# Optimization experiments

Measured on AMD Instinct MI355X. Metric: run time of the kernel, lower is better.

Reference implementation:

```python
import jax, jax.numpy as jnp
import numpy as np

K = 3
EPS = 1e-5
HID = 48
NB = 3


def conv2d(x, w, b):
    # x: NCHW, w: OIHW, 3x3 SAME conv stride 1
    y = jax.lax.conv_general_dilated(x, w, (1, 1), 'SAME',
                                     dimension_numbers=('NCHW', 'OIHW', 'NCHW'))
    return y + b[None, :, None, None]


def inorm(x):
    # InstanceNorm2d(affine=False): per-(n,c) spatial mean/var, biased var
    m = jnp.mean(x, axis=(2, 3), keepdims=True)
    v = jnp.var(x, axis=(2, 3), keepdims=True)
    return (x - m) * jax.lax.rsqrt(v + EPS)


def prelu(x, a):
    return jnp.where(x >= 0, x, a * x)


def basic_block(x, w, b, a):
    y = conv2d(x, w, b)
    y = inorm(y)
    y = prelu(y, a)
    y = inorm(y)
    return y + x


def maxpool2(x):
    n, c, h, w = x.shape
    return x.reshape(n, c, h // 2, 2, w // 2, 2).max(axis=(3, 5))


def upsample_bilinear8(x):
    # bilinear, scale_factor=8, align_corners=True
    n, c, h, w = x.shape
    H, W = h * 8, w * 8

    def coords(s, O):
        src = jnp.arange(O, dtype=jnp.float32) * (s - 1) / (O - 1)
        i0 = jnp.floor(src).astype(jnp.int32)
        i1 = jnp.minimum(i0 + 1, s - 1)
        return i0, i1, src - i0

    r0, r1, fr = coords(h, H)
    x = x[:, :, r0, :] * (1 - fr)[None, None, :, None] + x[:, :, r1, :] * fr[None, None, :, None]
    c0, c1, fc = coords(w, W)
    x = x[:, :, :, c0] * (1 - fc)[None, None, None, :] + x[:, :, :, c1] * fc[None, None, None, :]
    return x


def apply_kernel(x, kernel):
    # kernel: [n, k*k, h, w]; softmax over the k*k taps, reflect-pad unfold weighted sum
    kernel = jax.nn.softmax(kernel, axis=1)
    n, c, h, w = x.shape
    xp = jnp.pad(x, ((0, 0), (0, 0), (1, 1), (1, 1)), mode='reflect')
    patches = jnp.stack([xp[:, :, dy:dy + h, dx:dx + w]
                         for dy in range(K) for dx in range(K)], axis=0)  # [9,n,c,h,w]
    return jnp.einsum('pnchw,nphw->nchw', patches, kernel)


def setup_inputs() -> dict:
    key = jax.random.key(0)
    ks = jax.random.split(key, 12)
    f = jnp.float32
    inp = {
        'x': jax.random.normal(ks[0], (4, HID, 256, 256), dtype=f),
        'x_': jax.random.normal(ks[1], (4, HID, 256, 256), dtype=f),
        'pre1_w': jax.random.normal(ks[2], (NB, HID, HID, 3, 3), dtype=f) * 0.05,
        'pre1_b': jax.random.normal(ks[3], (NB, HID), dtype=f) * 0.05,
        'pre1_a': jnp.full((NB,), 0.25, dtype=f),
        'pre2_w': jax.random.normal(ks[4], (NB, HID, HID, 3, 3), dtype=f) * 0.05,
        'pre2_b': jax.random.normal(ks[5], (NB, HID), dtype=f) * 0.05,
        'pre2_a': jnp.full((NB,), 0.25, dtype=f),
        'prek_w1': jax.random.normal(ks[6], (HID, HID, 3, 3), dtype=f) * 0.05,
        'prek_b1': jax.random.normal(ks[7], (HID,), dtype=f) * 0.05,
        'prek_a': jnp.float32(0.25),
        'prek_w2': jax.random.normal(ks[8], (K * K, HID, 3, 3), dtype=f) * 0.05,
        'prek_b2': jax.random.normal(ks[9], (K * K,), dtype=f) * 0.05,
    }
    return inp


def reference(x, x_, pre1_w, pre1_b, pre1_a, pre2_w, pre2_b, pre2_a,
              prek_w1, prek_b1, prek_a, prek_w2, prek_b2):
    # F.interpolate(scale_factor=0.25, mode='nearest') == stride-4 subsample
    x1 = x_[:, :, ::4, ::4]
    for i in range(NB):
        x1 = basic_block(x1, pre1_w[i], pre1_b[i], pre1_a[i])
    x1 = maxpool2(x1)
    for i in range(NB):
        x1 = basic_block(x1, pre2_w[i], pre2_b[i], pre2_a[i])
    y = conv2d(x1, prek_w1, prek_b1)
    y = inorm(y)
    y = prelu(y, prek_a)
    skernel = conv2d(y, prek_w2, prek_b2)  # [n, k*k, H/8, W/8]
    kernel = upsample_bilinear8(skernel)   # [n, k*k, H, W]
    return apply_kernel(x, kernel)
```

## Files before the change

### kernel.cpp

```cpp
#include <hip/hip_runtime.h>
#include <cmath>

#define HIDC 48

__device__ __forceinline__ void block_meanvar1024(float s, float s2, float* red,
                                                  float cntinv, float& m, float& v)
{
#pragma unroll
    for (int off = 32; off > 0; off >>= 1) {
        s  += __shfl_down(s, off);
        s2 += __shfl_down(s2, off);
    }
    int wid  = threadIdx.x >> 6;
    int lane = threadIdx.x & 63;
    if (lane == 0) { red[wid] = s; red[16 + wid] = s2; }
    __syncthreads();
    if (threadIdx.x == 0) {
        float ts = 0.f, ts2 = 0.f;
#pragma unroll
        for (int i = 0; i < 16; ++i) { ts += red[i]; ts2 += red[16 + i]; }
        red[32] = ts; red[33] = ts2;
    }
    __syncthreads();
    float mean = red[32] * cntinv;
    m = mean;
    v = red[33] * cntinv - mean * mean;
    __syncthreads();
}

template <int H, int W, int ROWS, int COG, int CPS, int PXT, int NCH>
__global__ __launch_bounds__(ROWS*(W/PXT)) void conv_tile(
    const float* __restrict__ in,
    const float* __restrict__ wgt,
    float* __restrict__ out)
{
    constexpr int THREADS = ROWS * (W / PXT);
    constexpr int NPIX = H * W;
    constexpr int PW   = W + 4;
    constexpr int CHSZ = (ROWS + 2) * PW;
    constexpr int LSZ  = CPS * CHSZ;
    constexpr int TXN  = W / PXT;
    constexpr int NS   = NCH / CPS;
    constexpr int LPT  = (LSZ + THREADS - 1) / THREADS;

    __shared__ float plane[2][LSZ];

    const int t    = threadIdx.x;
    const int cg   = blockIdx.x;
    const int rt   = blockIdx.y;
    const int z    = blockIdx.z;
    const int half = z & 1;
    const int n    = z >> 1;
    const int COUT = gridDim.x * COG;
    const int co0  = cg * COG;
    const int cin0 = half * NCH;
    const int tx   = t % TXN;
    const int ty   = t / TXN;
    const int x0   = tx * PXT;
    const int r0   = rt * ROWS;
    const size_t OSTRIDE = (size_t)4 * COUT * NPIX;

    float acc[COG][PXT];
#pragma unroll
    for (int co = 0; co < COG; ++co)
#pragma unroll
        for (int p = 0; p < PXT; ++p) acc[co][p] = 0.f;

    const float* inb = in + ((size_t)n * 48 + cin0) * NPIX;

    int off[LPT];
#pragma unroll
    for (int k = 0; k < LPT; ++k) {
        int i = t + k * THREADS;
        off[k] = -1;
        if (i < LSZ) {
            int ch  = i / CHSZ;
            int rem = i % CHSZ;
            int ly  = rem / PW, lx = rem % PW;
            int gy  = r0 + ly - 1, gx = lx - 1;
            if (gy >= 0 && gy < H && gx >= 0 && gx < W)
                off[k] = ch * NPIX + gy * W + gx;
        }
    }

    float pref[LPT];
#pragma unroll
    for (int k = 0; k < LPT; ++k)
        pref[k] = (off[k] >= 0) ? inb[off[k]] : 0.f;

    int buf = 0;
    for (int s = 0; s < NS; ++s) {
        float cur[LPT];
#pragma unroll
        for (int k = 0; k < LPT; ++k) cur[k] = pref[k];
        if (s + 1 < NS) {
            const float* nb = inb + (size_t)(s + 1) * CPS * NPIX;
#pragma unroll
            for (int k = 0; k < LPT; ++k)
                pref[k] = (off[k] >= 0) ? nb[off[k]] : 0.f;
        }
#pragma unroll
        for (int k = 0; k < LPT; ++k) {
            int i = t + k * THREADS;
            if (i < LSZ) plane[buf][i] = cur[k];
        }
        __syncthreads();

#pragma unroll
        for (int c = 0; c < CPS; ++c) {
            const float* P = &plane[buf][c * CHSZ];
            float wv[COG][9];
#pragma unroll
            for (int co = 0; co < COG; ++co)
#pragma unroll
                for (int k = 0; k < 9; ++k)
                    wv[co][k] = wgt[((size_t)(co0 + co) * 48 + cin0 + s * CPS + c) * 9 + k];
            float vr[3][PXT + 2];
            if constexpr (PXT == 2) {
#pragma unroll
                for (int r = 0; r < 3; ++r) {
                    float2 a = *(const float2*)(P + (ty + r) * PW + x0);
                    float2 b = *(const float2*)(P + (ty + r) * PW + x0 + 2);
                    vr[r][0] = a.x; vr[r][1] = a.y; vr[r][2] = b.x; vr[r][3] = b.y;
                }
            } else {
#pragma unroll
                for (int r = 0; r < 3; ++r)
#pragma unroll
                    for (int j = 0; j < PXT + 2; ++j)
                        vr[r][j] = P[(ty + r) * PW + x0 + j];
            }
#pragma unroll
            for (int co = 0; co < COG; ++co)
#pragma unroll
                for (int p = 0; p < PXT; ++p) {
                    float s0 = vr[0][p]     * wv[co][0] + vr[0][p + 1] * wv[co][1]
                             + vr[0][p + 2] * wv[co][2] + vr[1][p]     * wv[co][3]
                             + vr[1][p + 1] * wv[co][4] + vr[1][p + 2] * wv[co][5]
                             + vr[2][p]     * wv[co][6] + vr[2][p + 1] * wv[co][7]
                             + vr[2][p + 2] * wv[co][8];
                    acc[co][p] += s0;
                }
        }
        buf ^= 1;
    }

#pragma unroll
    for (int co = 0; co < COG; ++co) {
        float* op = out + half * OSTRIDE
                  + (((size_t)n * COUT + co0 + co) * H + r0 + ty) * W + x0;
        if (PXT == 2) {
            *(float2*)op = make_float2(acc[co][0], acc[co][1]);
        } else {
#pragma unroll
            for (int p = 0; p < PXT; ++p) op[p] = acc[co][p];
        }
    }
}

template <int NPIX, int MODE, int POOL>
__global__ __launch_bounds__(1024) void norm_block(
    const float* __restrict__ c0,
    const float* __restrict__ c1,
    const float* __restrict__ res,
    const float* __restrict__ aptr,
    float* __restrict__ out)
{
    constexpr int TY = NPIX / 1024;
    constexpr bool VEC = (TY == 4) && (POOL == 0);
    __shared__ float red[34];
    const int t  = threadIdx.x;
    const int co = blockIdx.x;
    const int n  = blockIdx.y;
    const size_t base = ((size_t)n * 48 + co) * NPIX;
    constexpr float cntinv = 1.f / (float)NPIX;

    float acc[TY];
    size_t q = 0;
    if constexpr (POOL) {
        const int i = t >> 5, j = t & 31;
        q = base + (size_t)i * 128 + j * 2;
        float2 a0 = *(const float2*)(c0 + q);
        float2 a1 = *(const float2*)(c0 + q + 64);
        float2 b0 = *(const float2*)(c1 + q);
        float2 b1 = *(const float2*)(c1 + q + 64);
        acc[0] = a0.x + b0.x; acc[1] = a0.y + b0.y;
        acc[2] = a1.x + b1.x; acc[3] = a1.y + b1.y;
    } else if constexpr (VEC) {
        q = base + (size_t)t * 4;
        float4 a4 = *(const float4*)(c0 + q);
        float4 b4 = *(const float4*)(c1 + q);
        acc[0] = a4.x + b4.x; acc[1] = a4.y + b4.y;
        acc[2] = a4.z + b4.z; acc[3] = a4.w + b4.w;
    } else {
#pragma unroll
        for (int r = 0; r < TY; ++r)
            acc[r] = c0[base + t + r * 1024] + c1[base + t + r * 1024];
    }

    {
        float s = 0.f, s2 = 0.f;
#pragma unroll
        for (int r = 0; r < TY; ++r) { s += acc[r]; s2 += acc[r] * acc[r]; }
        float m, v;
        block_meanvar1024(s, s2, red, cntinv, m, v);
        float rr = rsqrtf(v + 1e-5f);
#pragma unroll
        for (int r = 0; r < TY; ++r) acc[r] = (acc[r] - m) * rr;
    }

    const float a = aptr[0];
#pragma unroll
    for (int r = 0; r < TY; ++r) acc[r] = acc[r] >= 0.f ? acc[r] : a * acc[r];

    if (MODE == 0) {
        float s = 0.f, s2 = 0.f;
#pragma unroll
        for (int r = 0; r < TY; ++r) { s += acc[r]; s2 += acc[r] * acc[r]; }
        float m, v;
        block_meanvar1024(s, s2, red, cntinv, m, v);
        float rr = rsqrtf(v + 1e-5f);
        if constexpr (POOL) {
            float2 r0v = *(const float2*)(res + q);
            float2 r1v = *(const float2*)(res + q + 64);
            acc[0] = (acc[0] - m) * rr + r0v.x;
            acc[1] = (acc[1] - m) * rr + r0v.y;
            acc[2] = (acc[2] - m) * rr + r1v.x;
            acc[3] = (acc[3] - m) * rr + r1v.y;
        } else if constexpr (VEC) {
            float4 r4 = *(const float4*)(res + q);
            acc[0] = (acc[0] - m) * rr + r4.x;
            acc[1] = (acc[1] - m) * rr + r4.y;
            acc[2] = (acc[2] - m) * rr + r4.z;
            acc[3] = (acc[3] - m) * rr + r4.w;
        } else {
#pragma unroll
            for (int r = 0; r < TY; ++r)
                acc[r] = (acc[r] - m) * rr + res[base + t + r * 1024];
        }
    }

    if constexpr (POOL) {
        out[(((size_t)n * 48 + co) << 10) + t] =
            fmaxf(fmaxf(acc[0], acc[1]), fmaxf(acc[2], acc[3]));
    } else if constexpr (VEC) {
        *(float4*)(out + q) = make_float4(acc[0], acc[1], acc[2], acc[3]);
    } else {
#pragma unroll
        for (int r = 0; r < TY; ++r) out[base + t + r * 1024] = acc[r];
    }
}

__global__ __launch_bounds__(256) void downsample4(const float* __restrict__ xin,
                                                   float* __restrict__ o)
{
    int idx = blockIdx.x * 256 + threadIdx.x;
    int j = idx & 63;
    int i = (idx >> 6) & 63;
    int nc = idx >> 12;
    o[idx] = xin[((size_t)nc * 256 + i * 4) * 256 + j * 4];
}

__global__ __launch_bounds__(256) void apply_fused(const float* __restrict__ x,
                                                   const float* __restrict__ sk0,
                                                   const float* __restrict__ sk1,
                                                   const float* __restrict__ kb2,
                                                   float* __restrict__ out)
{
    __shared__ float skr[9][2][32];
    __shared__ float kvs[9][256];
    const int bx = blockIdx.x;
    const int n  = bx >> 2;
    const int cg = bx & 3;
    const int h  = blockIdx.y;
    const int t  = threadIdx.x;

    const int wq = t & 63;
    const int cl = t >> 6;
    const int w4 = wq * 4;
    const int hm  = (h == 0) ? 1 : h - 1;
    const int hp  = (h == 255) ? 254 : h + 1;
    const int c0ch = cg * 12 + cl * 3;
    const float* xb = x + ((size_t)n * HIDC + c0ch) * 65536;
    float* ob = out + ((size_t)n * HIDC + c0ch) * 65536;

    float4 F[3][3];
#pragma unroll
    for (int c = 0; c < 3; ++c) {
        const float* xp = xb + (size_t)c * 65536;
        F[c][0] = *(const float4*)(xp + hm * 256 + w4);
        F[c][1] = *(const float4*)(xp + h  * 256 + w4);
        F[c][2] = *(const float4*)(xp + hp * 256 + w4);
    }

    float fs = (float)h * 31.0f / 255.0f;
    int r0 = (int)fs;
    float fh = fs - (float)r0;
    int r1 = min(r0 + 1, 31);

    for (int i = t; i < 576; i += 256) {
        int p = i >> 6, rsel = (i >> 5) & 1, c = i & 31;
        int rr = rsel ? r1 : r0;
        int idx = ((n * 9 + p) * 32 + rr) * 32 + c;
        skr[p][rsel][c] = sk0[idx] + sk1[idx] + kb2[p];
    }
    __syncthreads();

    {
        float fcs = (float)t * 31.0f / 255.0f;
        int c0 = (int)fcs;
        float fx = fcs - (float)c0;
        int c1 = min(c0 + 1, 31);
        float kv[9];
        float mx = -1e30f;
#pragma unroll
        for (int p = 0; p < 9; ++p) {
            float v0 = skr[p][0][c0] * (1.f - fx) + skr[p][0][c1] * fx;
            float v1 = skr[p][1][c0] * (1.f - fx) + skr[p][1][c1] * fx;
            float v  = v0 * (1.f - fh) + v1 * fh;
            kv[p] = v;
            mx = fmaxf(mx, v);
        }
        float ss = 0.f;
#pragma unroll
        for (int p = 0; p < 9; ++p) { kv[p] = __expf(kv[p] - mx); ss += kv[p]; }
        float inv = 1.f / ss;
#pragma unroll
        for (int p = 0; p < 9; ++p) kvs[p][t] = kv[p] * inv;
    }
    __syncthreads();

    float kv[4][9];
#pragma unroll
    for (int p = 0; p < 9; ++p) {
        float4 v = *(const float4*)&kvs[p][w4];
        kv[0][p] = v.x; kv[1][p] = v.y; kv[2][p] = v.z; kv[3][p] = v.w;
    }

#pragma unroll
    for (int c = 0; c < 3; ++c) {
        float4 fm = F[c][0];
        float4 fc = F[c][1];
        float4 fp = F[c][2];
        float lm = __shfl_up(fm.w, 1);   if (wq == 0)  lm = fm.y;
        float lc = __shfl_up(fc.w, 1);   if (wq == 0)  lc = fc.y;
        float lp = __shfl_up(fp.w, 1);   if (wq == 0)  lp = fp.y;
        float rmr = __shfl_down(fm.x, 1); if (wq == 63) rmr = fm.z;
        float rcr = __shfl_down(fc.x, 1); if (wq == 63) rcr = fc.z;
        float rpr = __shfl_down(fp.x, 1); if (wq == 63) rpr = fp.z;
        float vm[6] = { lm, fm.x, fm.y, fm.z, fm.w, rmr };
        float vc[6] = { lc, fc.x, fc.y, fc.z, fc.w, rcr };
        float vp[6] = { lp, fp.x, fp.y, fp.z, fp.w, rpr };
        float4 o;
        float* op = &o.x;
#pragma unroll
        for (int j = 0; j < 4; ++j) {
            op[j] = kv[j][0] * vm[j] + kv[j][1] * vm[j + 1] + kv[j][2] * vm[j + 2]
                  + kv[j][3] * vc[j] + kv[j][4] * vc[j + 1] + kv[j][5] * vc[j + 2]
                  + kv[j][6] * vp[j] + kv[j][7] * vp[j + 1] + kv[j][8] * vp[j + 2];
        }
        *(float4*)(ob + (size_t)c * 65536 + h * 256 + w4) = o;
    }
}

extern "C" void kernel_launch(void* const* d_in, const int* in_sizes, int n_in,
                              void* d_out, int out_size, void* d_ws, size_t ws_size,
                              hipStream_t stream)
{
    (void)in_sizes; (void)n_in; (void)out_size; (void)ws_size;
    const float* x       = (const float*)d_in[0];
    const float* x_      = (const float*)d_in[1];
    const float* pre1_w  = (const float*)d_in[2];
    const float* pre1_a  = (const float*)d_in[4];
    const float* pre2_w  = (const float*)d_in[5];
    const float* pre2_a  = (const float*)d_in[7];
    const float* prek_w1 = (const float*)d_in[8];
    const float* prek_a  = (const float*)d_in[10];
    const float* prek_w2 = (const float*)d_in[11];
    const float* prek_b2 = (const float*)d_in[12];
    float* out = (float*)d_out;

    float* A   = (float*)d_ws;
    float* B   = A + 786432;
    float* R0  = B + 786432;
    float* R1  = R0 + 786432;
    float* C   = R1 + 786432;
    float* D   = C + 196608;
    float* SK0 = D + 196608;
    float* SK1 = SK0 + 36864;

    const int W1 = 48 * 48 * 9;

    downsample4<<<3072, 256, 0, stream>>>(x_, A);

    conv_tile<64, 64, 4, 3, 2, 2, 24><<<dim3(16, 16, 8), 128, 0, stream>>>(A, pre1_w, R0);
    norm_block<4096, 0, 0><<<dim3(48, 4), 1024, 0, stream>>>(R0, R1, A, pre1_a, B);
    conv_tile<64, 64, 4, 3, 2, 2, 24><<<dim3(16, 16, 8), 128, 0, stream>>>(B, pre1_w + W1, R0);
    norm_block<4096, 0, 0><<<dim3(48, 4), 1024, 0, stream>>>(R0, R1, B, pre1_a + 1, A);
    conv_tile<64, 64, 4, 3, 2, 2, 24><<<dim3(16, 16, 8), 128, 0, stream>>>(A, pre1_w + 2 * W1, R0);
    norm_block<4096, 0, 1><<<dim3(48, 4), 1024, 0, stream>>>(R0, R1, A, pre1_a + 2, C);

    conv_tile<32, 32, 4, 2, 4, 1, 24><<<dim3(24, 8, 8), 128, 0, stream>>>(C, pre2_w, R0);
    norm_block<1024, 0, 0><<<dim3(48, 4), 1024, 0, stream>>>(R0, R0 + 196608, C, pre2_a, D);
    conv_tile<32, 32, 4, 2, 4, 1, 24><<<dim3(24, 8, 8), 128, 0, stream>>>(D, pre2_w + W1, R0);
    norm_block<1024, 0, 0><<<dim3(48, 4), 1024, 0, stream>>>(R0, R0 + 196608, D, pre2_a + 1, C);
    conv_tile<32, 32, 4, 2, 4, 1, 24><<<dim3(24, 8, 8), 128, 0, stream>>>(C, pre2_w + 2 * W1, R0);
    norm_block<1024, 0, 0><<<dim3(48, 4), 1024, 0, stream>>>(R0, R0 + 196608, C, pre2_a + 2, D);

    conv_tile<32, 32, 4, 2, 4, 1, 24><<<dim3(24, 8, 8), 128, 0, stream>>>(D, prek_w1, R0);
    norm_block<1024, 1, 0><<<dim3(48, 4), 1024, 0, stream>>>(R0, R0 + 196608, nullptr, prek_a, C);
    conv_tile<32, 32, 4, 3, 4, 1, 24><<<dim3(3, 8, 8), 128, 0, stream>>>(C, prek_w2, SK0);

    apply_fused<<<dim3(16, 256), 256, 0, stream>>>(x, SK0, SK1, prek_b2, out);
}
```

Baseline: 303.2 us.

## Process four output rows per block in apply kernel and reorder conv grid

The final apply kernel now computes four consecutive output rows per block and loads a six-row input window per channel, so each row's neighbour rows are reused from registers instead of being re-read from global memory. The softmax kernel weights for all four rows are precomputed into shared memory. Separately, the conv grid is reordered so the batch/half index sits in blockIdx.x and the output-channel group in blockIdx.z, with COUT made a template constant. This raises register and shared-memory use per block and reduces the number of blocks in the apply kernel.

New measurement: 303.9 us. About the same (+0.2%).

```diff
diff --git a/kernel.cpp b/kernel.cpp
--- a/kernel.cpp
+++ b/kernel.cpp
@@ -28,7 +28,7 @@
     __syncthreads();
 }
 
-template <int H, int W, int ROWS, int COG, int CPS, int PXT, int NCH>
+template <int H, int W, int ROWS, int COG, int CPS, int PXT, int NCH, int COUT>
 __global__ __launch_bounds__(ROWS*(W/PXT)) void conv_tile(
     const float* __restrict__ in,
     const float* __restrict__ wgt,
@@ -46,12 +46,11 @@
     __shared__ float plane[2][LSZ];
 
     const int t    = threadIdx.x;
-    const int cg   = blockIdx.x;
+    const int z    = blockIdx.x;
     const int rt   = blockIdx.y;
-    const int z    = blockIdx.z;
+    const int cg   = blockIdx.z;
     const int half = z & 1;
     const int n    = z >> 1;
-    const int COUT = gridDim.x * COG;
     const int co0  = cg * COG;
     const int cin0 = half * NCH;
     const int tx   = t % TXN;
@@ -267,40 +266,38 @@
                                                    const float* __restrict__ kb2,
                                                    float* __restrict__ out)
 {
-    __shared__ float skr[9][2][32];
-    __shared__ float kvs[9][256];
+    __shared__ float skr[9][3][32];
+    __shared__ float kvs[4][9][256];
     const int bx = blockIdx.x;
     const int n  = bx >> 2;
     const int cg = bx & 3;
-    const int h  = blockIdx.y;
+    const int h0 = blockIdx.y * 4;
     const int t  = threadIdx.x;
 
     const int wq = t & 63;
     const int cl = t >> 6;
     const int w4 = wq * 4;
-    const int hm  = (h == 0) ? 1 : h - 1;
-    const int hp  = (h == 255) ? 254 : h + 1;
     const int c0ch = cg * 12 + cl * 3;
     const float* xb = x + ((size_t)n * HIDC + c0ch) * 65536;
     float* ob = out + ((size_t)n * HIDC + c0ch) * 65536;
 
-    float4 F[3][3];
+    float4 F[3][6];
 #pragma unroll
     for (int c = 0; c < 3; ++c) {
         const float* xp = xb + (size_t)c * 65536;
-        F[c][0] = *(const float4*)(xp + hm * 256 + w4);
-        F[c][1] = *(const float4*)(xp + h  * 256 + w4);
-        F[c][2] = *(const float4*)(xp + hp * 256 + w4);
-    }
-
-    float fs = (float)h * 31.0f / 255.0f;
-    int r0 = (int)fs;
-    float fh = fs - (float)r0;
-    int r1 = min(r0 + 1, 31);
-
-    for (int i = t; i < 576; i += 256) {
-        int p = i >> 6, rsel = (i >> 5) & 1, c = i & 31;
-        int rr = rsel ? r1 : r0;
+#pragma unroll
+        for (int k = 0; k < 6; ++k) {
+            int g = h0 - 1 + k;
+            g = (g < 0) ? 1 : (g > 255 ? 254 : g);
+            F[c][k] = *(const float4*)(xp + g * 256 + w4);
+        }
+    }
+
+    const int r_0 = (h0 * 31) / 255;
+    for (int i = t; i < 864; i += 256) {
+        int p = i / 96, rem = i % 96;
+        int rsel = rem >> 5, c = rem & 31;
+        int rr = min(r_0 + rsel, 31);
         int idx = ((n * 9 + p) * 32 + rr) * 32 + c;
         skr[p][rsel][c] = sk0[idx] + sk1[idx] + kb2[p];
     }
@@ -311,55 +308,65 @@
         int c0 = (int)fcs;
         float fx = fcs - (float)c0;
         int c1 = min(c0 + 1, 31);
-        float kv[9];
-        float mx = -1e30f;
+#pragma unroll
+        for (int ro = 0; ro < 4; ++ro) {
+            float fs = (float)(h0 + ro) * 31.0f / 255.0f;
+            int rh = (int)fs;
+            float fh = fs - (float)rh;
+            int a_ = rh - r_0;
+            int b_ = a_ + 1;
+            float kv[9];
+            float mx = -1e30f;
+#pragma unroll
+            for (int p = 0; p < 9; ++p) {
+                float v0 = skr[p][a_][c0] * (1.f - fx) + skr[p][a_][c1] * fx;
+                float v1 = skr[p][b_][c0] * (1.f - fx) + skr[p][b_][c1] * fx;
+                float v  = v0 * (1.f - fh) + v1 * fh;
+                kv[p] = v;
+                mx = fmaxf(mx, v);
+            }
+            float ss = 0.f;
+#pragma unroll
+            for (int p = 0; p < 9; ++p) { kv[p] = __expf(kv[p] - mx); ss += kv[p]; }
+            float inv = 1.f / ss;
+#pragma unroll
+            for (int p = 0; p < 9; ++p) kvs[ro][p][t] = kv[p] * inv;
+        }
+    }
+    __syncthreads();
+
+#pragma unroll
+    for (int ro = 0; ro < 4; ++ro) {
+        float kv[4][9];
 #pragma unroll
         for (int p = 0; p < 9; ++p) {
-            float v0 = skr[p][0][c0] * (1.f - fx) + skr[p][0][c1] * fx;
-            float v1 = skr[p][1][c0] * (1.f - fx) + skr[p][1][c1] * fx;
-            float v  = v0 * (1.f - fh) + v1 * fh;
-            kv[p] = v;
-            mx = fmaxf(mx, v);
-        }
-        float ss = 0.f;
-#pragma unroll
-        for (int p = 0; p < 9; ++p) { kv[p] = __expf(kv[p] - mx); ss += kv[p]; }
-        float inv = 1.f / ss;
-#pragma unroll
-        for (int p = 0; p < 9; ++p) kvs[p][t] = kv[p] * inv;
-    }
-    __syncthreads();
-
-    float kv[4][9];
-#pragma unroll
-    for (int p = 0; p < 9; ++p) {
-        float4 v = *(const float4*)&kvs[p][w4];
-        kv[0][p] = v.x; kv[1][p] = v.y; kv[2][p] = v.z; kv[3][p] = v.w;
-    }
-
-#pragma unroll
-    for (int c = 0; c < 3; ++c) {
-        float4 fm = F[c][0];
-        float4 fc = F[c][1];
-        float4 fp = F[c][2];
-        float lm = __shfl_up(fm.w, 1);   if (wq == 0)  lm = fm.y;
-        float lc = __shfl_up(fc.w, 1);   if (wq == 0)  lc = fc.y;
-        float lp = __shfl_up(fp.w, 1);   if (wq == 0)  lp = fp.y;
-        float rmr = __shfl_down(fm.x, 1); if (wq == 63) rmr = fm.z;
-        float rcr = __shfl_down(fc.x, 1); if (wq == 63) rcr = fc.z;
-        float rpr = __shfl_down(fp.x, 1); if (wq == 63) rpr = fp.z;
-        float vm[6] = { lm, fm.x, fm.y, fm.z, fm.w, rmr };
-        float vc[6] = { lc, fc.x, fc.y, fc.z, fc.w, rcr };
-        float vp[6] = { lp, fp.x, fp.y, fp.z, fp.w, rpr };
-        float4 o;
-        float* op = &o.x;
-#pragma unroll
-        for (int j = 0; j < 4; ++j) {
-            op[j] = kv[j][0] * vm[j] + kv[j][1] * vm[j + 1] + kv[j][2] * vm[j + 2]
-                  + kv[j][3] * vc[j] + kv[j][4] * vc[j + 1] + kv[j][5] * vc[j + 2]
-                  + kv[j][6] * vp[j] + kv[j][7] * vp[j + 1] + kv[j][8] * vp[j + 2];
-        }
-        *(float4*)(ob + (size_t)c * 65536 + h * 256 + w4) = o;
+            float4 v = *(const float4*)&kvs[ro][p][w4];
+            kv[0][p] = v.x; kv[1][p] = v.y; kv[2][p] = v.z; kv[3][p] = v.w;
+        }
+#pragma unroll
+        for (int c = 0; c < 3; ++c) {
+            float4 fm = F[c][ro];
+            float4 fc = F[c][ro + 1];
+            float4 fp = F[c][ro + 2];
+            float lm = __shfl_up(fm.w, 1);   if (wq == 0)  lm = fm.y;
+            float lc = __shfl_up(fc.w, 1);   if (wq == 0)  lc = fc.y;
+            float lp = __shfl_up(fp.w, 1);   if (wq == 0)  lp = fp.y;
+            float rmr = __shfl_down(fm.x, 1); if (wq == 63) rmr = fm.z;
+            float rcr = __shfl_down(fc.x, 1); if (wq == 63) rcr = fc.z;
+            float rpr = __shfl_down(fp.x, 1); if (wq == 63) rpr = fp.z;
+            float vm[6] = { lm, fm.x, fm.y, fm.z, fm.w, rmr };
+            float vc[6] = { lc, fc.x, fc.y, fc.z, fc.w, rcr };
+            float vp[6] = { lp, fp.x, fp.y, fp.z, fp.w, rpr };
+            float4 o;
+            float* op = &o.x;
+#pragma unroll
+            for (int j = 0; j < 4; ++j) {
+                op[j] = kv[j][0] * vm[j] + kv[j][1] * vm[j + 1] + kv[j][2] * vm[j + 2]
+                      + kv[j][3] * vc[j] + kv[j][4] * vc[j + 1] + kv[j][5] * vc[j + 2]
+                      + kv[j][6] * vp[j] + kv[j][7] * vp[j + 1] + kv[j][8] * vp[j + 2];
+            }
+            *(float4*)(ob + (size_t)c * 65536 + (h0 + ro) * 256 + w4) = o;
+        }
     }
 }
 
@@ -393,23 +400,23 @@
 
     downsample4<<<3072, 256, 0, stream>>>(x_, A);
 
-    conv_tile<64, 64, 4, 3, 2, 2, 24><<<dim3(16, 16, 8), 128, 0, stream>>>(A, pre1_w, R0);
+    conv_tile<64, 64, 4, 3, 2, 2, 24, 48><<<dim3(8, 16, 16), 128, 0, stream>>>(A, pre1_w, R0);
     norm_block<4096, 0, 0><<<dim3(48, 4), 1024, 0, stream>>>(R0, R1, A, pre1_a, B);
-    conv_tile<64, 64, 4, 3, 2, 2, 24><<<dim3(16, 16, 8), 128, 0, stream>>>(B, pre1_w + W1, R0);
+    conv_tile<64, 64, 4, 3, 2, 2, 24, 48><<<dim3(8, 16, 16), 128, 0, stream>>>(B, pre1_w + W1, R0);
     norm_block<4096, 0, 0><<<dim3(48, 4), 1024, 0, stream>>>(R0, R1, B, pre1_a + 1, A);
-    conv_tile<64, 64, 4, 3, 2, 2, 24><<<dim3(16, 16, 8), 128, 0, stream>>>(A, pre1_w + 2 * W1, R0);
+    conv_tile<64, 64, 4, 3, 2, 2, 24, 48><<<dim3(8, 16, 16), 128, 0, stream>>>(A, pre1_w + 2 * W1, R0);
     norm_block<4096, 0, 1><<<dim3(48, 4), 1024, 0, stream>>>(R0, R1, A, pre1_a + 2, C);
 
-    conv_tile<32, 32, 4, 2, 4, 1, 24><<<dim3(24, 8, 8), 128, 0, stream>>>(C, pre2_w, R0);
+    conv_tile<32, 32, 4, 2, 4, 1, 24, 48><<<dim3(8, 8, 24), 128, 0, stream>>>(C, pre2_w, R0);
     norm_block<1024, 0, 0><<<dim3(48, 4), 1024, 0, stream>>>(R0, R0 + 196608, C, pre2_a, D);
-    conv_tile<32, 32, 4, 2, 4, 1, 24><<<dim3(24, 8, 8), 128, 0, stream>>>(D, pre2_w + W1, R0);
+    conv_tile<32, 32, 4, 2, 4, 1, 24, 48><<<dim3(8, 8, 24), 128, 0, stream>>>(D, pre2_w + W1, R0);
     norm_block<1024, 0, 0><<<dim3(48, 4), 1024, 0, stream>>>(R0, R0 + 196608, D, pre2_a + 1, C);
-    conv_tile<32, 32, 4, 2, 4, 1, 24><<<dim3(24, 8, 8), 128, 0, stream>>>(C, pre2_w + 2 * W1, R0);
+    conv_tile<32, 32, 4, 2, 4, 1, 24, 48><<<dim3(8, 8, 24), 128, 0, stream>>>(C, pre2_w + 2 * W1, R0);
     norm_block<1024, 0, 0><<<dim3(48, 4), 1024, 0, stream>>>(R0, R0 + 196608, C, pre2_a + 2, D);
 
-    conv_tile<32, 32, 4, 2, 4, 1, 24><<<dim3(24, 8, 8), 128, 0, stream>>>(D, prek_w1, R0);
+    conv_tile<32, 32, 4, 2, 4, 1, 24, 48><<<dim3(8, 8, 24), 128, 0, stream>>>(D, prek_w1, R0);
     norm_block<1024, 1, 0><<<dim3(48, 4), 1024, 0, stream>>>(R0, R0 + 196608, nullptr, prek_a, C);
-    conv_tile<32, 32, 4, 3, 4, 1, 24><<<dim3(3, 8, 8), 128, 0, stream>>>(C, prek_w2, SK0);
-
-    apply_fused<<<dim3(16, 256), 256, 0, stream>>>(x, SK0, SK1, prek_b2, out);
-}
+    conv_tile<32, 32, 4, 3, 4, 1, 24, 9><<<dim3(8, 8, 3), 128, 0, stream>>>(C, prek_w2, SK0);
+
+    apply_fused<<<dim3(16, 64), 256, 0, stream>>>(x, SK0, SK1, prek_b2, out);
+}
```
